# Kernel tuning notes

Measured on AMD Instinct MI355X. Metric: run time of the kernel, lower is better.

The kernel has to match this reference:

```python
import jax, jax.numpy as jnp
import numpy as np


def _calc_square_dist(a, b):
    # a: [B,N,C], b: [B,M,C] -> [B,N,M] squared euclidean distance (norm=False)
    a2 = jnp.sum(a * a, axis=-1)            # [B,N]
    b2 = jnp.sum(b * b, axis=-1)            # [B,M]
    ab = jnp.einsum('bnc,bmc->bnm', a, b)   # [B,N,M]
    return a2[:, :, None] + b2[:, None, :] - 2.0 * ab


def _furthest_point_sample_with_dist(dist, npoint):
    # dist: [B,N,N]; classic FPS: start at index 0, maintain min-dist to the
    # selected set, pick argmax each step. Sequential over npoint via lax.scan.
    B, N, _ = dist.shape
    mind = dist[:, 0, :]  # min distance to selected set {0}: [B,N]

    def step(mind, _):
        far = jnp.argmax(mind, axis=1).astype(jnp.int32)              # [B]
        d = jnp.take_along_axis(dist, far[:, None, None], axis=1)     # [B,1,N]
        mind = jnp.minimum(mind, d[:, 0, :])
        return mind, far

    _, idxs = jax.lax.scan(step, mind, None, length=npoint - 1)  # [npoint-1, B]
    idxs = jnp.concatenate([jnp.zeros((1, B), jnp.int32), idxs], axis=0)
    return idxs.T  # [B, npoint]


def setup_inputs() -> dict:
    key = jax.random.key(0)
    k1, k2 = jax.random.split(key)
    B, N, C = 2, 8192, 64
    points = jax.random.normal(k1, (B, N, 3), dtype=jnp.float32)
    features = jax.random.normal(k2, (B, C, N), dtype=jnp.float32)
    return {"points": points, "features": features, "npoint": 1024}


def reference(points, features, npoint):
    # F-FPS: concat xyz with per-point features, pairwise sq-dist, FPS on dist.
    feats_for_fps = jnp.concatenate(
        [points, jnp.transpose(features, (0, 2, 1))], axis=2)  # [B,N,3+C]
    features_dist = _calc_square_dist(feats_for_fps, feats_for_fps)  # [B,N,N]
    fps_idx = _furthest_point_sample_with_dist(features_dist, npoint)
    return fps_idx
```

## Files before the change

kernel.cpp:

```cpp
#include <hip/hip_runtime.h>

#define BB    2
#define NN    8192
#define CC    64
#define NPT   1024
#define NT    128
#define NBLK  16
#define TPB   512

__device__ __forceinline__ unsigned int fkey(float v) {
  unsigned int u = __float_as_uint(v);
  return (u & 0x80000000u) ? ~u : (u | 0x80000000u);
}

__device__ __forceinline__ unsigned wave_max_u32(unsigned x) {
  int v = (int)x, t;
  t = __builtin_amdgcn_update_dpp(v, v, 0x111, 0xf, 0xf, false);
  v = ((unsigned)t > (unsigned)v) ? t : v;
  t = __builtin_amdgcn_update_dpp(v, v, 0x112, 0xf, 0xf, false);
  v = ((unsigned)t > (unsigned)v) ? t : v;
  t = __builtin_amdgcn_update_dpp(v, v, 0x114, 0xf, 0xf, false);
  v = ((unsigned)t > (unsigned)v) ? t : v;
  t = __builtin_amdgcn_update_dpp(v, v, 0x118, 0xf, 0xf, false);
  v = ((unsigned)t > (unsigned)v) ? t : v;
  t = __builtin_amdgcn_update_dpp(v, v, 0x142, 0xa, 0xf, false);
  v = ((unsigned)t > (unsigned)v) ? t : v;
  t = __builtin_amdgcn_update_dpp(v, v, 0x143, 0xc, 0xf, false);
  v = ((unsigned)t > (unsigned)v) ? t : v;
  return (unsigned)__builtin_amdgcn_readlane(v, 63);
}

__global__ __launch_bounds__(256) void dist_kernel(
    const float* __restrict__ Pb,
    const float* __restrict__ Fb,
    float* __restrict__ Db) {
  __shared__ __align__(16) float Ai[67][64];
  __shared__ __align__(16) float Aj[67][64];
  __shared__ float ni_s[64], nj_s[64];
  const int bid = blockIdx.x;
  const int bi  = bid >> 7, bj = bid & (NT - 1);
  const int t   = threadIdx.x;
  const int i0  = bi * 64, j0 = bj * 64;

  for (int idx = t; idx < 67 * 64; idx += 256) {
    const int c = idx >> 6, r = idx & 63;
    float vi, vj;
    if (c < 3) {
      vi = Pb[(size_t)(i0 + r) * 3 + c];
      vj = Pb[(size_t)(j0 + r) * 3 + c];
    } else {
      vi = Fb[(size_t)(c - 3) * NN + i0 + r];
      vj = Fb[(size_t)(c - 3) * NN + j0 + r];
    }
    Ai[c][r] = vi;
    Aj[c][r] = vj;
  }
  __syncthreads();

  if (t < 64) {
    float n = 0.f;
#pragma unroll
    for (int k = 0; k < 67; ++k) n = fmaf(Ai[k][t], Ai[k][t], n);
    ni_s[t] = n;
  } else if (t < 128) {
    const int r = t - 64;
    float n = 0.f;
#pragma unroll
    for (int k = 0; k < 67; ++k) n = fmaf(Aj[k][r], Aj[k][r], n);
    nj_s[r] = n;
  }
  __syncthreads();

  const int tx = t & 15, ty = t >> 4;
  float acc[4][4] = {};
  for (int k = 0; k < 67; ++k) {
    const float4 a = *(const float4*)&Ai[k][ty * 4];
    const float4 v = *(const float4*)&Aj[k][tx * 4];
    acc[0][0] = fmaf(a.x, v.x, acc[0][0]); acc[0][1] = fmaf(a.x, v.y, acc[0][1]);
    acc[0][2] = fmaf(a.x, v.z, acc[0][2]); acc[0][3] = fmaf(a.x, v.w, acc[0][3]);
    acc[1][0] = fmaf(a.y, v.x, acc[1][0]); acc[1][1] = fmaf(a.y, v.y, acc[1][1]);
    acc[1][2] = fmaf(a.y, v.z, acc[1][2]); acc[1][3] = fmaf(a.y, v.w, acc[1][3]);
    acc[2][0] = fmaf(a.z, v.x, acc[2][0]); acc[2][1] = fmaf(a.z, v.y, acc[2][1]);
    acc[2][2] = fmaf(a.z, v.z, acc[2][2]); acc[2][3] = fmaf(a.z, v.w, acc[2][3]);
    acc[3][0] = fmaf(a.w, v.x, acc[3][0]); acc[3][1] = fmaf(a.w, v.y, acc[3][1]);
    acc[3][2] = fmaf(a.w, v.z, acc[3][2]); acc[3][3] = fmaf(a.w, v.w, acc[3][3]);
  }

  const float4 nj4 = *(const float4*)&nj_s[tx * 4];
#pragma unroll
  for (int r = 0; r < 4; ++r) {
    const float nir = ni_s[ty * 4 + r];
    float4 w;
    w.x = (nir + nj4.x) - 2.0f * acc[r][0];
    w.y = (nir + nj4.y) - 2.0f * acc[r][1];
    w.z = (nir + nj4.z) - 2.0f * acc[r][2];
    w.w = (nir + nj4.w) - 2.0f * acc[r][3];
    *(float4*)&Db[(size_t)(i0 + ty * 4 + r) * NN + j0 + tx * 4] = w;
  }
}

__global__ __launch_bounds__(512) void scan_kernel(
    const float* __restrict__ D, unsigned long long dstride,
    int* __restrict__ out, int ostride) {
  const int b = blockIdx.x;
  const float* Db = D + (size_t)b * dstride;
  int* ob = out + (size_t)b * ostride;
  const int tid = threadIdx.x, lane = tid & 63;
  __shared__ unsigned long long slot[3];
  if (tid < 3) slot[tid] = 0ull;
  __syncthreads();

  float4 m[4];
#pragma unroll
  for (int k = 0; k < 4; ++k) m[k] = make_float4(3.0e38f, 3.0e38f, 3.0e38f, 3.0e38f);

  if (tid == 0) ob[0] = 0;
  int far = 0;

  for (int s = 1; s < NPT; ++s) {
    const float4* row4 = (const float4*)(Db + (size_t)far * NN);
    float4 v[4];
#pragma unroll
    for (int k = 0; k < 4; ++k) v[k] = row4[tid + 512 * k];
#pragma unroll
    for (int k = 0; k < 4; ++k) {
      m[k].x = fminf(m[k].x, v[k].x);
      m[k].y = fminf(m[k].y, v[k].y);
      m[k].z = fminf(m[k].z, v[k].z);
      m[k].w = fminf(m[k].w, v[k].w);
    }

    const int j0 = tid * 4;
    float best = m[0].x; int bj = j0;
#define CHK(val, jj) if ((val) > best) { best = (val); bj = (jj); }
    CHK(m[0].y, j0 + 1) CHK(m[0].z, j0 + 2) CHK(m[0].w, j0 + 3)
    CHK(m[1].x, j0 + 2048) CHK(m[1].y, j0 + 2049) CHK(m[1].z, j0 + 2050) CHK(m[1].w, j0 + 2051)
    CHK(m[2].x, j0 + 4096) CHK(m[2].y, j0 + 4097) CHK(m[2].z, j0 + 4098) CHK(m[2].w, j0 + 4099)
    CHK(m[3].x, j0 + 6144) CHK(m[3].y, j0 + 6145) CHK(m[3].z, j0 + 6146) CHK(m[3].w, j0 + 6147)
#undef CHK

    const unsigned fk   = fkey(best);
    const unsigned wmax = wave_max_u32(fk);
    const unsigned cand = (fk == wmax) ? (8191u - (unsigned)bj) : 0u;
    const unsigned wtie = wave_max_u32(cand);

    if (lane == 0)
      atomicMax(&slot[s % 3], ((unsigned long long)wmax << 32) | wtie);
    if (tid == 0) slot[(s + 1) % 3] = 0ull;
    __syncthreads();

    const unsigned long long g = slot[s % 3];
    far = 8191 - (int)(g & 0x1FFFu);
    if (tid == 0) ob[s] = far;
  }
}


#define R64(M) \
  M(0) M(1) M(2) M(3) M(4) M(5) M(6) M(7) \
  M(8) M(9) M(10) M(11) M(12) M(13) M(14) M(15) \
  M(16) M(17) M(18) M(19) M(20) M(21) M(22) M(23) \
  M(24) M(25) M(26) M(27) M(28) M(29) M(30) M(31) \
  M(32) M(33) M(34) M(35) M(36) M(37) M(38) M(39) \
  M(40) M(41) M(42) M(43) M(44) M(45) M(46) M(47) \
  M(48) M(49) M(50) M(51) M(52) M(53) M(54) M(55) \
  M(56) M(57) M(58) M(59) M(60) M(61) M(62) M(63)

__global__ __attribute__((amdgpu_waves_per_eu(1, 2))) __launch_bounds__(TPB)
void fps_fallback(const float* __restrict__ pts, const float* __restrict__ feat,
                  int* __restrict__ out, unsigned long long* __restrict__ slots) {
  const int blk  = blockIdx.x & (NBLK - 1);
  const int b    = blockIdx.x >> 4;
  const int tid  = threadIdx.x;
  const int lane = tid & 63;
  const int p    = blk * TPB + tid;

  const float* Pp = pts  + (size_t)b * NN * 3 + (size_t)p * 3;
  const float* Fp = feat + (size_t)b * CC * NN + p;

  float fx = Pp[0], fy = Pp[1], fz = Pp[2];
#define DCF(i) float fc##i = Fp[(i) * NN];
  R64(DCF)
#undef DCF
  asm volatile("" : "+v"(fx), "+v"(fy), "+v"(fz));
#define PIN(i) asm volatile("" : "+v"(fc##i));
  R64(PIN)
#undef PIN

  float nrm = 0.f;
  nrm += fx * fx; nrm += fy * fy; nrm += fz * fz;
#define NR(i) nrm += fc##i * fc##i;
  R64(NR)
#undef NR

  __shared__ unsigned long long wred[TPB / 64];
  __shared__ int far_sh;

  if (blk == 0 && tid == 0) out[b * NPT] = 0;

  float mind = 3.0e38f;
  int far = 0;

  for (int s = 1; s < NPT; ++s) {
    const int fu = __builtin_amdgcn_readfirstlane(far);
    const float* Pq = pts  + (size_t)b * NN * 3 + (size_t)fu * 3;
    const float* Fq = feat + (size_t)b * CC * NN + fu;
    const float gx = Pq[0], gy = Pq[1], gz = Pq[2];
#define GL(i) const float gc##i = Fq[(i) * NN];
    R64(GL)
#undef GL
    float nf = 0.f, dot = 0.f;
    nf += gx * gx; nf += gy * gy; nf += gz * gz;
#define NF(i) nf += gc##i * gc##i;
    R64(NF)
#undef NF
    dot += fx * gx; dot += fy * gy; dot += fz * gz;
#define DT(i) dot += fc##i * gc##i;
    R64(DT)
#undef DT
    const float d = (nf + nrm) - 2.0f * dot;
    mind = fminf(mind, d);

    unsigned long long key =
        ((unsigned long long)fkey(mind) << 13) | (unsigned int)(8191 - p);
#pragma unroll
    for (int off = 1; off < 64; off <<= 1) {
      unsigned long long o = __shfl_xor(key, off);
      key = key > o ? key : o;
    }
    if (lane == 0) wred[tid >> 6] = key;
    __syncthreads();

    if (tid < 64) {
      unsigned long long bk = wred[0];
#pragma unroll
      for (int w = 1; w < TPB / 64; ++w) bk = bk > wred[w] ? bk : wred[w];
      unsigned long long* sb = slots + ((size_t)(s & 1) * BB + b) * NBLK;
      if (tid == 0) {
        bk |= ((unsigned long long)s << 45);
        __hip_atomic_store(&sb[blk], bk, __ATOMIC_RELAXED, __HIP_MEMORY_SCOPE_AGENT);
      }
      unsigned long long v = 0;
      for (;;) {
        if (tid < NBLK)
          v = __hip_atomic_load(&sb[tid], __ATOMIC_RELAXED, __HIP_MEMORY_SCOPE_AGENT);
        const bool ok = (tid < NBLK) ? ((v >> 45) == (unsigned long long)s) : true;
        if (__all(ok)) break;
        __builtin_amdgcn_s_sleep(1);
      }
#pragma unroll
      for (int off = 8; off; off >>= 1) {
        unsigned long long o = __shfl_xor(v, off);
        v = v > o ? v : o;
      }
      if (tid == 0) far_sh = 8191 - (int)(v & 0x1FFFu);
    }
    __syncthreads();
    far = far_sh;
    if (blk == 0 && tid == 0) out[b * NPT + s] = far;
  }
}


extern "C" void kernel_launch(void* const* d_in, const int* in_sizes, int n_in,
                              void* d_out, int out_size, void* d_ws, size_t ws_size,
                              hipStream_t stream) {
  const float* pts  = (const float*)d_in[0];
  const float* feat = (const float*)d_in[1];
  int* out = (int*)d_out;

  const size_t oneD = (size_t)NN * NN * sizeof(float);
  if (ws_size >= 2 * oneD) {
    float* D = (float*)d_ws;
    for (int b = 0; b < BB; ++b)
      dist_kernel<<<NT * NT, 256, 0, stream>>>(
          pts + (size_t)b * NN * 3, feat + (size_t)b * CC * NN, D + (size_t)b * NN * NN);
    scan_kernel<<<BB, 512, 0, stream>>>(D, (unsigned long long)NN * NN, out, NPT);
  } else if (ws_size >= oneD) {
    float* D = (float*)d_ws;
    for (int b = 0; b < BB; ++b) {
      dist_kernel<<<NT * NT, 256, 0, stream>>>(
          pts + (size_t)b * NN * 3, feat + (size_t)b * CC * NN, D);
      scan_kernel<<<1, 512, 0, stream>>>(D, 0, out + (size_t)b * NPT, 0);
    }
  } else {
    unsigned long long* slots = (unsigned long long*)d_ws;
    hipMemsetAsync(d_ws, 0, 2 * BB * NBLK * sizeof(unsigned long long), stream);
    void* args[] = {(void*)&pts, (void*)&feat, (void*)&out, (void*)&slots};
    dim3 grid(BB * NBLK), block(TPB);
    hipLaunchCooperativeKernel((void*)fps_fallback, grid, block, args, 0, stream);
  }
}
```

Before: 2.191 ms.

## Speculatively prefetch runner-up row and replace atomic slot with per-wave reduction

The FPS scan loop now stores each wave's packed max in a shared array and reduces all eight entries redundantly in every thread, instead of doing an atomicMax into a rotating slot. It also finds the second-best wave candidate and prefetches that distance row into a spare register set, so that if the next step's winner matches the prediction the dependent row load is already in flight. The prediction only works when the next argmax equals the current runner-up wave's candidate. Otherwise the row is fetched again, and the extra loads per step add memory traffic and register pressure.

```diff
diff --git a/kernel.cpp b/kernel.cpp
--- a/kernel.cpp
+++ b/kernel.cpp
@@ -99,60 +99,93 @@
   }
 }
 
-__global__ __launch_bounds__(512) void scan_kernel(
-    const float* __restrict__ D, unsigned long long dstride,
-    int* __restrict__ out, int ostride) {
+
+#define CHK(val, jj) if ((val) > best) { best = (val); bj = (jj); }
+
+#define SCAN_STEP(C0,C1,C2,C3, predC, P0,P1,P2,P3, predP, s)                   \
+  {                                                                            \
+    if (far != predC) {    \
+      const float4* r4_ = (const float4*)(Db + (size_t)far * NN);              \
+      C0 = r4_[tid]; C1 = r4_[tid + 512];                                      \
+      C2 = r4_[tid + 1024]; C3 = r4_[tid + 1536];                              \
+    }                                                                          \
+    m0.x = fminf(m0.x, C0.x); m0.y = fminf(m0.y, C0.y);                        \
+    m0.z = fminf(m0.z, C0.z); m0.w = fminf(m0.w, C0.w);                        \
+    m1.x = fminf(m1.x, C1.x); m1.y = fminf(m1.y, C1.y);                        \
+    m1.z = fminf(m1.z, C1.z); m1.w = fminf(m1.w, C1.w);                        \
+    m2.x = fminf(m2.x, C2.x); m2.y = fminf(m2.y, C2.y);                        \
+    m2.z = fminf(m2.z, C2.z); m2.w = fminf(m2.w, C2.w);                        \
+    m3.x = fminf(m3.x, C3.x); m3.y = fminf(m3.y, C3.y);                        \
+    m3.z = fminf(m3.z, C3.z); m3.w = fminf(m3.w, C3.w);                        \
+    const int j0_ = tid * 4;                                                   \
+    float best = m0.x; int bj = j0_;                                           \
+    CHK(m0.y, j0_ + 1) CHK(m0.z, j0_ + 2) CHK(m0.w, j0_ + 3)                   \
+    CHK(m1.x, j0_ + 2048) CHK(m1.y, j0_ + 2049)                                \
+    CHK(m1.z, j0_ + 2050) CHK(m1.w, j0_ + 2051)                                \
+    CHK(m2.x, j0_ + 4096) CHK(m2.y, j0_ + 4097)                                \
+    CHK(m2.z, j0_ + 4098) CHK(m2.w, j0_ + 4099)                                \
+    CHK(m3.x, j0_ + 6144) CHK(m3.y, j0_ + 6145)                                \
+    CHK(m3.z, j0_ + 6146) CHK(m3.w, j0_ + 6147)                                \
+    const unsigned fk_   = fkey(best);                                         \
+    const unsigned wmax_ = wave_max_u32(fk_);                                  \
+    const unsigned cand_ = (fk_ == wmax_) ? (8191u - (unsigned)bj) : 0u;       \
+    const unsigned wtie_ = wave_max_u32(cand_);                                \
+    if (lane == 0)                                                             \
+      wred[(s) & 1][wid] = ((unsigned long long)wmax_ << 32) | wtie_;          \
+    __syncthreads();         \
+    const unsigned long long* W_ = wred[(s) & 1];                              \
+    const unsigned long long g0_=W_[0], g1_=W_[1], g2_=W_[2], g3_=W_[3],       \
+                             g4_=W_[4], g5_=W_[5], g6_=W_[6], g7_=W_[7];       \
+    unsigned long long h0_ = g0_>g1_?g0_:g1_, h1_ = g2_>g3_?g2_:g3_;           \
+    unsigned long long h2_ = g4_>g5_?g4_:g5_, h3_ = g6_>g7_?g6_:g7_;           \
+    unsigned long long q0_ = h0_>h1_?h0_:h1_, q1_ = h2_>h3_?h2_:h3_;           \
+    const unsigned long long win_ = q0_>q1_?q0_:q1_;                           \
+    far = 8191 - (int)(win_ & 0x1FFFu);                                        \
+    if (tid == 0) ob[s] = far;                                                 \
+               \
+    unsigned long long e0_ = g0_==win_?0ull:g0_, e1_ = g1_==win_?0ull:g1_;     \
+    unsigned long long e2_ = g2_==win_?0ull:g2_, e3_ = g3_==win_?0ull:g3_;     \
+    unsigned long long e4_ = g4_==win_?0ull:g4_, e5_ = g5_==win_?0ull:g5_;     \
+    unsigned long long e6_ = g6_==win_?0ull:g6_, e7_ = g7_==win_?0ull:g7_;     \
+    e0_ = e0_>e1_?e0_:e1_; e2_ = e2_>e3_?e2_:e3_;                              \
+    e4_ = e4_>e5_?e4_:e5_; e6_ = e6_>e7_?e6_:e7_;                              \
+    e0_ = e0_>e2_?e0_:e2_; e4_ = e4_>e6_?e4_:e6_;                              \
+    const unsigned long long sec_ = e0_>e4_?e0_:e4_;                           \
+    const int nrun_ = 8191 - (int)(sec_ & 0x1FFFu);                            \
+                       \
+    {                                                                          \
+      const float4* p4_ = (const float4*)(Db + (size_t)nrun_ * NN);            \
+      P0 = p4_[tid]; P1 = p4_[tid + 512];                                      \
+      P2 = p4_[tid + 1024]; P3 = p4_[tid + 1536];                              \
+      predP = nrun_;                                                           \
+    }                                                                          \
+  }
+
+__global__ __attribute__((amdgpu_waves_per_eu(1, 2))) __launch_bounds__(512)
+void scan_kernel(const float* __restrict__ D, unsigned long long dstride,
+                 int* __restrict__ out, int ostride) {
   const int b = blockIdx.x;
   const float* Db = D + (size_t)b * dstride;
   int* ob = out + (size_t)b * ostride;
-  const int tid = threadIdx.x, lane = tid & 63;
-  __shared__ unsigned long long slot[3];
-  if (tid < 3) slot[tid] = 0ull;
-  __syncthreads();
-
-  float4 m[4];
-#pragma unroll
-  for (int k = 0; k < 4; ++k) m[k] = make_float4(3.0e38f, 3.0e38f, 3.0e38f, 3.0e38f);
+  const int tid = threadIdx.x, lane = tid & 63, wid = tid >> 6;
+  __shared__ unsigned long long wred[2][8];
+
+  float4 m0 = make_float4(3.0e38f, 3.0e38f, 3.0e38f, 3.0e38f);
+  float4 m1 = m0, m2 = m0, m3 = m0;
+  float4 A0, A1, A2, A3, B0, B1, B2, B3;
+  int far = 0, predA = -1, predB = -1;
 
   if (tid == 0) ob[0] = 0;
-  int far = 0;
-
-  for (int s = 1; s < NPT; ++s) {
-    const float4* row4 = (const float4*)(Db + (size_t)far * NN);
-    float4 v[4];
-#pragma unroll
-    for (int k = 0; k < 4; ++k) v[k] = row4[tid + 512 * k];
-#pragma unroll
-    for (int k = 0; k < 4; ++k) {
-      m[k].x = fminf(m[k].x, v[k].x);
-      m[k].y = fminf(m[k].y, v[k].y);
-      m[k].z = fminf(m[k].z, v[k].z);
-      m[k].w = fminf(m[k].w, v[k].w);
-    }
-
-    const int j0 = tid * 4;
-    float best = m[0].x; int bj = j0;
-#define CHK(val, jj) if ((val) > best) { best = (val); bj = (jj); }
-    CHK(m[0].y, j0 + 1) CHK(m[0].z, j0 + 2) CHK(m[0].w, j0 + 3)
-    CHK(m[1].x, j0 + 2048) CHK(m[1].y, j0 + 2049) CHK(m[1].z, j0 + 2050) CHK(m[1].w, j0 + 2051)
-    CHK(m[2].x, j0 + 4096) CHK(m[2].y, j0 + 4097) CHK(m[2].z, j0 + 4098) CHK(m[2].w, j0 + 4099)
-    CHK(m[3].x, j0 + 6144) CHK(m[3].y, j0 + 6145) CHK(m[3].z, j0 + 6146) CHK(m[3].w, j0 + 6147)
-#undef CHK
-
-    const unsigned fk   = fkey(best);
-    const unsigned wmax = wave_max_u32(fk);
-    const unsigned cand = (fk == wmax) ? (8191u - (unsigned)bj) : 0u;
-    const unsigned wtie = wave_max_u32(cand);
-
-    if (lane == 0)
-      atomicMax(&slot[s % 3], ((unsigned long long)wmax << 32) | wtie);
-    if (tid == 0) slot[(s + 1) % 3] = 0ull;
-    __syncthreads();
-
-    const unsigned long long g = slot[s % 3];
-    far = 8191 - (int)(g & 0x1FFFu);
-    if (tid == 0) ob[s] = far;
-  }
+
+  int s = 1;
+#pragma unroll 1
+  for (int pair = 0; pair < (NPT - 2) / 2; ++pair) {
+    SCAN_STEP(A0, A1, A2, A3, predA, B0, B1, B2, B3, predB, s)
+    ++s;
+    SCAN_STEP(B0, B1, B2, B3, predB, A0, A1, A2, A3, predA, s)
+    ++s;
+  }
+  SCAN_STEP(A0, A1, A2, A3, predA, B0, B1, B2, B3, predB, s)
 }
 
 
```

After: 3.198 ms. 1.46x slower.
